# Optimization experiments

Measured on AMD Instinct MI355X. Metric: run time of the kernel, lower is better.

## Reference

```python
import jax, jax.numpy as jnp
import numpy as np

D_MODEL = 1024
NUM_HEADS = 16
HEAD_SIZE = D_MODEL // NUM_HEADS  # 64; used ONLY as the softmax scale (module never splits heads)


def setup_inputs() -> dict:
    key = jax.random.key(0)
    ks = jax.random.split(key, 7)
    B, L, D = 4, 2048, D_MODEL
    q = jax.random.normal(ks[0], (B, L, D), dtype=jnp.float32)
    k = jax.random.normal(ks[1], (B, L, D), dtype=jnp.float32)
    v = jax.random.normal(ks[2], (B, L, D), dtype=jnp.float32)
    s = 1.0 / np.sqrt(D)
    Wq = jax.random.uniform(ks[3], (D, D), jnp.float32, -s, s)
    Wk = jax.random.uniform(ks[4], (D, D), jnp.float32, -s, s)
    Wv = jax.random.uniform(ks[5], (D, D), jnp.float32, -s, s)
    Wproj = jax.random.uniform(ks[6], (D, D), jnp.float32, -s, s)
    return {"q": q, "k": k, "v": v, "Wq": Wq, "Wk": Wk, "Wv": Wv, "Wproj": Wproj}


def reference(q, k, v, Wq, Wk, Wv, Wproj):
    # nn.Linear(x) = x @ W.T; weights stored [out, in]
    L = q.shape[1]
    qh = jnp.einsum('bld,ed->ble', q, Wq)
    kh = jnp.einsum('bld,ed->ble', k, Wk)
    vh = jnp.einsum('bld,ed->ble', v, Wv)
    # NOTE: module attends over the full d_model channel (no head split),
    # but scales by head_size ** -0.5 — faithful to the source.
    att = jnp.einsum('bqd,bkd->bqk', qh, kh) * (HEAD_SIZE ** -0.5)
    causal = jnp.tril(jnp.ones((L, L), dtype=bool))  # bias buffer
    att = jnp.where(causal, att, -jnp.inf)
    att = jax.nn.softmax(att, axis=-1)
    y = jnp.einsum('bqk,bkd->bqd', att, vh)
    y = jnp.einsum('bld,ed->ble', y, Wproj)
    return y
```

## Files before the change

### kernel.cpp

```cpp
#include <hip/hip_runtime.h>
#include <hip/hip_bf16.h>
#include <stdint.h>

typedef __bf16 bf16x8 __attribute__((ext_vector_type(8)));
typedef float  f32x4  __attribute__((ext_vector_type(4)));

__device__ __forceinline__ unsigned short f2bf(float f) {
  unsigned int u = __float_as_uint(f);
  u += 0x7FFF + ((u >> 16) & 1);
  return (unsigned short)(u >> 16);
}

#define BM 128
#define BN 128
#define BK 32

#define GLOAD_LDS(gptr, ldsptr)                                                     \
  __builtin_amdgcn_global_load_lds(                                                 \
      (const __attribute__((address_space(1))) unsigned int*)(gptr),                \
      (__attribute__((address_space(3))) unsigned int*)(ldsptr), 16, 0, 0)

__global__ __launch_bounds__(256, 2) void gemm_bt(
    const unsigned short* __restrict__ A,
    const unsigned short* __restrict__ B,
    void* __restrict__ C,
    int M, int N, int K, int ntiles,
    long sAz, long sBz, long sCz,
    int mode, int causal_skip, int klimit, float scale)
{
  const int nwg  = gridDim.x;
  const int orig = blockIdx.x;
  const int qq = nwg >> 3, rr = nwg & 7, xc = orig & 7, oo = orig >> 3;
  const int wg = (xc < rr ? xc * (qq + 1) : rr * (qq + 1) + (xc - rr) * qq) + oo;
  const int mt = wg / ntiles, nt = wg % ntiles;
  const int z  = blockIdx.y;
  if (causal_skip && nt > mt) return;
  const int emode = (mode == 3) ? (z == 2 ? 1 : 0) : mode;

  A += sAz * (long)z;
  B += sBz * (long)z;

  __shared__ __align__(16) unsigned short As[2][BM * BK];
  __shared__ __align__(16) unsigned short Bs[2][BN * BK];

  const int tid  = threadIdx.x;
  const int wave = tid >> 6;
  const int lane = tid & 63;
  const int wr = wave >> 1, wc = wave & 1;

  f32x4 acc[4][4];
#pragma unroll
  for (int i = 0; i < 4; ++i)
#pragma unroll
    for (int j = 0; j < 4; ++j) acc[i][j] = (f32x4){0.f, 0.f, 0.f, 0.f};

  int kiters = K / BK;
  if (klimit) { int kl = (mt + 1) * BM; if (kl < K) kiters = kl / BK; }

  const int r0 = tid >> 2, s0 = tid & 3;
  const int c0 = ((s0 ^ ((r0 >> 1) & 3)) << 3);
  const int r1 = r0 + 64;
  const int c1 = ((s0 ^ ((r1 >> 1) & 3)) << 3);
  const long aoff0 = (long)(mt * BM + r0) * K + c0;
  const long aoff1 = (long)(mt * BM + r1) * K + c1;
  const long boff0 = (long)(nt * BN + r0) * K + c0;
  const long boff1 = (long)(nt * BN + r1) * K + c1;
  const unsigned ldsw = wave * 1024;

#define STAGE(bi, k0)                                                     \
  do {                                                                    \
    GLOAD_LDS(A + aoff0 + (k0), (char*)&As[bi][0]    + ldsw);             \
    GLOAD_LDS(A + aoff1 + (k0), (char*)&As[bi][2048] + ldsw);             \
    GLOAD_LDS(B + boff0 + (k0), (char*)&Bs[bi][0]    + ldsw);             \
    GLOAD_LDS(B + boff1 + (k0), (char*)&Bs[bi][2048] + ldsw);             \
  } while (0)

  STAGE(0, 0);

  int cur = 0;
  for (int kt = 0; kt < kiters; ++kt) {
    if (kt + 1 < kiters) {
      STAGE(cur ^ 1, (kt + 1) * BK);
      asm volatile("s_waitcnt vmcnt(4)" ::: "memory");
    } else {
      asm volatile("s_waitcnt vmcnt(0)" ::: "memory");
    }
    __builtin_amdgcn_s_barrier();
    asm volatile("" ::: "memory");

    bf16x8 af[4], bfr[4];
#pragma unroll
    for (int i = 0; i < 4; ++i) {
      const int ar = wr * 64 + i * 16 + (lane & 15);
      const int as = ((lane >> 4) ^ ((ar >> 1) & 3)) << 3;
      af[i] = *(const bf16x8*)&As[cur][ar * BK + as];
      const int br = wc * 64 + i * 16 + (lane & 15);
      const int bs = ((lane >> 4) ^ ((br >> 1) & 3)) << 3;
      bfr[i] = *(const bf16x8*)&Bs[cur][br * BK + bs];
    }
#pragma unroll
    for (int mi = 0; mi < 4; ++mi)
#pragma unroll
      for (int ni = 0; ni < 4; ++ni)
        acc[mi][ni] = __builtin_amdgcn_mfma_f32_16x16x32_bf16(af[mi], bfr[ni], acc[mi][ni], 0, 0, 0);

    asm volatile("" ::: "memory");
    __builtin_amdgcn_s_barrier();
    cur ^= 1;
  }
#undef STAGE

  const int rb = mt * BM + wr * 64;
  const int cb = nt * BN + wc * 64;

  if (emode == 0) {
    unsigned short* Cb = (unsigned short*)C + sCz * (long)z;
#pragma unroll
    for (int mi = 0; mi < 4; ++mi)
#pragma unroll
      for (int ni = 0; ni < 4; ++ni) {
        const int row0 = rb + mi * 16 + ((lane >> 4) << 2);
        const int col  = cb + ni * 16 + (lane & 15);
#pragma unroll
        for (int j = 0; j < 4; ++j)
          Cb[(long)(row0 + j) * N + col] = f2bf(acc[mi][ni][j]);
      }
  } else if (emode == 1) {
    unsigned short* Cb = (unsigned short*)C + sCz * (long)z;
#pragma unroll
    for (int mi = 0; mi < 4; ++mi)
#pragma unroll
      for (int ni = 0; ni < 4; ++ni) {
        const int row0 = rb + mi * 16 + ((lane >> 4) << 2);
        const int col  = cb + ni * 16 + (lane & 15);
#pragma unroll
        for (int j = 0; j < 4; ++j) {
          const int row = row0 + j;
          const int b = row >> 11, l = row & 2047;
          Cb[((long)b * N + col) * 2048 + l] = f2bf(acc[mi][ni][j]);
        }
      }
  } else {
    float* Cf = (float*)C + sCz * (long)z;
#pragma unroll
    for (int mi = 0; mi < 4; ++mi)
#pragma unroll
      for (int ni = 0; ni < 4; ++ni) {
        const int row0 = rb + mi * 16 + ((lane >> 4) << 2);
        const int col  = cb + ni * 16 + (lane & 15);
#pragma unroll
        for (int j = 0; j < 4; ++j)
          Cf[(long)(row0 + j) * N + col] = acc[mi][ni][j] * scale;
      }
  }
}

__global__ __launch_bounds__(256) void f32_to_bf16_vec(
    const float* __restrict__ src, unsigned short* __restrict__ dst, long nvec4)
{
  long i = (long)blockIdx.x * 256 + threadIdx.x;
  const long stride = (long)gridDim.x * 256;
  for (; i < nvec4; i += stride) {
    float4 v = ((const float4*)src)[i];
    ushort4 o;
    o.x = f2bf(v.x); o.y = f2bf(v.y); o.z = f2bf(v.z); o.w = f2bf(v.w);
    ((ushort4*)dst)[i] = o;
  }
}

__global__ __launch_bounds__(256) void softmax_causal(
    const float* __restrict__ S, unsigned short* __restrict__ P, int L)
{
  const int r = blockIdx.x;
  const int b = r >> 11, q = r & 2047;
  const float* srow = S + ((long)b * L + q) * L;
  unsigned short* prow = P + ((long)b * L + q) * L;
  const int len = q + 1;
  const int tid = threadIdx.x, lane = tid & 63, wave = tid >> 6;
  __shared__ float red[8];

  float m = -3.4e38f;
  for (int i = tid; i < len; i += 256) m = fmaxf(m, srow[i]);
#pragma unroll
  for (int o = 32; o; o >>= 1) m = fmaxf(m, __shfl_xor(m, o));
  if (lane == 0) red[wave] = m;
  __syncthreads();
  m = fmaxf(fmaxf(red[0], red[1]), fmaxf(red[2], red[3]));

  float s = 0.f;
  for (int i = tid; i < len; i += 256) s += __expf(srow[i] - m);
#pragma unroll
  for (int o = 32; o; o >>= 1) s += __shfl_xor(s, o);
  if (lane == 0) red[4 + wave] = s;
  __syncthreads();
  s = (red[4] + red[5]) + (red[6] + red[7]);
  const float inv = 1.f / s;

  for (int i = tid; i < L; i += 256) {
    unsigned short o16 = 0;
    if (i < len) o16 = f2bf(__expf(srow[i] - m) * inv);
    prow[i] = o16;
  }
}

extern "C" void kernel_launch(void* const* d_in, const int* in_sizes, int n_in,
                              void* d_out, int out_size, void* d_ws, size_t ws_size,
                              hipStream_t stream) {
  const float* q  = (const float*)d_in[0];
  const float* k  = (const float*)d_in[1];
  const float* v  = (const float*)d_in[2];
  const float* Wq = (const float*)d_in[3];
  const float* Wk = (const float*)d_in[4];
  const float* Wv = (const float*)d_in[5];
  const float* Wp = (const float*)d_in[6];
  float* out = (float*)d_out;

  const long D    = 1024;
  const long L    = 2048;
  const long ND   = 8192 * D;
  const long NS   = 4L * L * L;

  char* ws = (char*)d_ws;
  unsigned short* qh    = (unsigned short*)ws;
  unsigned short* kh    = qh  + ND;
  unsigned short* vhT   = kh  + ND;
  unsigned short* P     = vhT + ND;
  unsigned short* ybf   = P   + NS;
  unsigned short* wbf   = ybf + ND;
  float*          S     = (float*)(wbf + 4L * D * D);
  unsigned short* qkvbf = (unsigned short*)S;

  f32_to_bf16_vec<<<2048, 256, 0, stream>>>(q,  qkvbf,           ND / 4);
  f32_to_bf16_vec<<<2048, 256, 0, stream>>>(k,  qkvbf + ND,      ND / 4);
  f32_to_bf16_vec<<<2048, 256, 0, stream>>>(v,  qkvbf + 2 * ND,  ND / 4);
  f32_to_bf16_vec<<<512,  256, 0, stream>>>(Wq, wbf,                 D * D / 4);
  f32_to_bf16_vec<<<512,  256, 0, stream>>>(Wk, wbf + D * D,         D * D / 4);
  f32_to_bf16_vec<<<512,  256, 0, stream>>>(Wv, wbf + 2 * D * D,     D * D / 4);
  f32_to_bf16_vec<<<512,  256, 0, stream>>>(Wp, wbf + 3 * D * D,     D * D / 4);

  gemm_bt<<<dim3(512, 3), 256, 0, stream>>>(qkvbf, wbf, qh,
      8192, 1024, 1024, 8, ND, D * D, ND, 3, 0, 0, 1.0f);

  gemm_bt<<<dim3(256, 4), 256, 0, stream>>>(qh, kh, S,
      2048, 2048, 1024, 16, L * D, L * D, L * L, 2, 1, 0, 0.125f);

  softmax_causal<<<8192, 256, 0, stream>>>(S, P, 2048);

  gemm_bt<<<dim3(128, 4), 256, 0, stream>>>(P, vhT, ybf,
      2048, 1024, 2048, 8, L * L, D * L, L * D, 0, 0, 1, 1.0f);

  gemm_bt<<<dim3(512, 1), 256, 0, stream>>>(ybf, wbf + 3 * D * D, out,
      8192, 1024, 1024, 8, 0, 0, 0, 2, 0, 0, 1.0f);
}
```

Measured before the change: 250.4 us.

## Triple-buffer GEMM loads, fuse conversion launches, vectorize causal softmax

The GEMM kernel moves from double to triple LDS buffering, prefetching two K-steps ahead with adjusted waitcnts, and its launch-bounds occupancy hint rises from 2 to 3. The seven f32-to-bf16 conversion launches are merged into one kernel that dispatches on block index. The softmax now has each thread load its 8 row elements once into registers, reuse them for max, exp and sum, and write one 16-byte vector, so the row is read once instead of three times. The extra LDS buffer raises shared memory per block, which could limit occupancy, and the softmax now hardcodes L=2048 with 256 threads.

```diff
diff --git a/kernel.cpp b/kernel.cpp
--- a/kernel.cpp
+++ b/kernel.cpp
@@ -4,6 +4,7 @@
 
 typedef __bf16 bf16x8 __attribute__((ext_vector_type(8)));
 typedef float  f32x4  __attribute__((ext_vector_type(4)));
+typedef unsigned short ushort8v __attribute__((ext_vector_type(8)));
 
 __device__ __forceinline__ unsigned short f2bf(float f) {
   unsigned int u = __float_as_uint(f);
@@ -20,7 +21,7 @@
       (const __attribute__((address_space(1))) unsigned int*)(gptr),                \
       (__attribute__((address_space(3))) unsigned int*)(ldsptr), 16, 0, 0)
 
-__global__ __launch_bounds__(256, 2) void gemm_bt(
+__global__ __launch_bounds__(256, 3) void gemm_bt(
     const unsigned short* __restrict__ A,
     const unsigned short* __restrict__ B,
     void* __restrict__ C,
@@ -40,8 +41,8 @@
   A += sAz * (long)z;
   B += sBz * (long)z;
 
-  __shared__ __align__(16) unsigned short As[2][BM * BK];
-  __shared__ __align__(16) unsigned short Bs[2][BN * BK];
+  __shared__ __align__(16) unsigned short As[3][BM * BK];
+  __shared__ __align__(16) unsigned short Bs[3][BN * BK];
 
   const int tid  = threadIdx.x;
   const int wave = tid >> 6;
@@ -76,11 +77,16 @@
   } while (0)
 
   STAGE(0, 0);
+  if (kiters > 1) STAGE(1, BK);
 
   int cur = 0;
   for (int kt = 0; kt < kiters; ++kt) {
-    if (kt + 1 < kiters) {
-      STAGE(cur ^ 1, (kt + 1) * BK);
+    const int rem = kiters - 1 - kt;
+    if (rem >= 2) {
+      int sb = cur + 2; if (sb >= 3) sb -= 3;
+      STAGE(sb, (kt + 2) * BK);
+      asm volatile("s_waitcnt vmcnt(8)" ::: "memory");
+    } else if (rem == 1) {
       asm volatile("s_waitcnt vmcnt(4)" ::: "memory");
     } else {
       asm volatile("s_waitcnt vmcnt(0)" ::: "memory");
@@ -106,7 +112,7 @@
 
     asm volatile("" ::: "memory");
     __builtin_amdgcn_s_barrier();
-    cur ^= 1;
+    cur = (cur == 2) ? 0 : cur + 1;
   }
 #undef STAGE
 
@@ -155,15 +161,31 @@
   }
 }
 
-__global__ __launch_bounds__(256) void f32_to_bf16_vec(
-    const float* __restrict__ src, unsigned short* __restrict__ dst, long nvec4)
+__global__ __launch_bounds__(256) void convert_all(
+    const float* __restrict__ q, const float* __restrict__ k, const float* __restrict__ v,
+    const float* __restrict__ wq, const float* __restrict__ wk,
+    const float* __restrict__ wv, const float* __restrict__ wp,
+    unsigned short* __restrict__ qkv, unsigned short* __restrict__ wb)
 {
-  long i = (long)blockIdx.x * 256 + threadIdx.x;
-  const long stride = (long)gridDim.x * 256;
-  for (; i < nvec4; i += stride) {
-    float4 v = ((const float4*)src)[i];
+  const long NQ = 8192L * 1024 / 4;
+  const long NW = 1024L * 1024 / 4;
+  const int blk = blockIdx.x;
+  const float* src; unsigned short* dst; long n; int nb, bb;
+  if (blk < 1536) {
+    const int s = blk >> 9;
+    src = (s == 0) ? q : (s == 1) ? k : v;
+    dst = qkv + (long)s * (8192L * 1024);
+    n = NQ; nb = 512; bb = blk & 511;
+  } else {
+    const int s = (blk - 1536) >> 6;
+    src = (s == 0) ? wq : (s == 1) ? wk : (s == 2) ? wv : wp;
+    dst = wb + (long)s * (1024L * 1024);
+    n = NW; nb = 64; bb = (blk - 1536) & 63;
+  }
+  for (long i = (long)bb * 256 + threadIdx.x; i < n; i += (long)nb * 256) {
+    float4 x = ((const float4*)src)[i];
     ushort4 o;
-    o.x = f2bf(v.x); o.y = f2bf(v.y); o.z = f2bf(v.z); o.w = f2bf(v.w);
+    o.x = f2bf(x.x); o.y = f2bf(x.y); o.z = f2bf(x.z); o.w = f2bf(x.w);
     ((ushort4*)dst)[i] = o;
   }
 }
@@ -177,18 +199,28 @@
   unsigned short* prow = P + ((long)b * L + q) * L;
   const int len = q + 1;
   const int tid = threadIdx.x, lane = tid & 63, wave = tid >> 6;
+  const int base = tid * 8;
   __shared__ float red[8];
 
+  float4 x0 = ((const float4*)srow)[tid * 2];
+  float4 x1 = ((const float4*)srow)[tid * 2 + 1];
+  float vv[8] = {x0.x, x0.y, x0.z, x0.w, x1.x, x1.y, x1.z, x1.w};
+
   float m = -3.4e38f;
-  for (int i = tid; i < len; i += 256) m = fmaxf(m, srow[i]);
+#pragma unroll
+  for (int i = 0; i < 8; ++i) if (base + i < len) m = fmaxf(m, vv[i]);
 #pragma unroll
   for (int o = 32; o; o >>= 1) m = fmaxf(m, __shfl_xor(m, o));
   if (lane == 0) red[wave] = m;
   __syncthreads();
   m = fmaxf(fmaxf(red[0], red[1]), fmaxf(red[2], red[3]));
 
-  float s = 0.f;
-  for (int i = tid; i < len; i += 256) s += __expf(srow[i] - m);
+  float p[8], s = 0.f;
+#pragma unroll
+  for (int i = 0; i < 8; ++i) {
+    p[i] = (base + i < len) ? __expf(vv[i] - m) : 0.f;
+    s += p[i];
+  }
 #pragma unroll
   for (int o = 32; o; o >>= 1) s += __shfl_xor(s, o);
   if (lane == 0) red[4 + wave] = s;
@@ -196,11 +228,10 @@
   s = (red[4] + red[5]) + (red[6] + red[7]);
   const float inv = 1.f / s;
 
-  for (int i = tid; i < L; i += 256) {
-    unsigned short o16 = 0;
-    if (i < len) o16 = f2bf(__expf(srow[i] - m) * inv);
-    prow[i] = o16;
-  }
+  ushort8v o16;
+#pragma unroll
+  for (int i = 0; i < 8; ++i) o16[i] = f2bf(p[i] * inv);
+  *(ushort8v*)(prow + base) = o16;
 }
 
 extern "C" void kernel_launch(void* const* d_in, const int* in_sizes, int n_in,
@@ -230,13 +261,7 @@
   float*          S     = (float*)(wbf + 4L * D * D);
   unsigned short* qkvbf = (unsigned short*)S;
 
-  f32_to_bf16_vec<<<2048, 256, 0, stream>>>(q,  qkvbf,           ND / 4);
-  f32_to_bf16_vec<<<2048, 256, 0, stream>>>(k,  qkvbf + ND,      ND / 4);
-  f32_to_bf16_vec<<<2048, 256, 0, stream>>>(v,  qkvbf + 2 * ND,  ND / 4);
-  f32_to_bf16_vec<<<512,  256, 0, stream>>>(Wq, wbf,                 D * D / 4);
-  f32_to_bf16_vec<<<512,  256, 0, stream>>>(Wk, wbf + D * D,         D * D / 4);
-  f32_to_bf16_vec<<<512,  256, 0, stream>>>(Wv, wbf + 2 * D * D,     D * D / 4);
-  f32_to_bf16_vec<<<512,  256, 0, stream>>>(Wp, wbf + 3 * D * D,     D * D / 4);
+  convert_all<<<1792, 256, 0, stream>>>(q, k, v, Wq, Wk, Wv, Wp, qkvbf, wbf);
 
   gemm_bt<<<dim3(512, 3), 256, 0, stream>>>(qkvbf, wbf, qh,
       8192, 1024, 1024, 8, ND, D * D, ND, 3, 0, 0, 1.0f);
```

New measurement: 238.2 us. 1.05x faster.
